# Performance work log

Hardware: AMD Instinct MI355X
Metric: run time of the kernel (lower is better)

## Reference

```python
import jax, jax.numpy as jnp
import numpy as np

B, S, T, D, V = 512, 128, 128, 512, 128  # batch, enc len, dec steps (=longest_smi), dim_model, output_size


def setup_inputs() -> dict:
    key = jax.random.key(0)
    ks = jax.random.split(key, 17)
    sc = 0.05
    return {
        "e_all": jax.random.normal(ks[0], (B, S, D), jnp.float32),
        "e_h": jax.random.normal(ks[1], (1, B, D), jnp.float32),
        "e_c": jax.random.normal(ks[2], (1, B, D), jnp.float32),
        "target": jax.random.randint(ks[3], (B, T), 0, T),
        # params (Linear weights stored [in, out], y = x @ W + b)
        "E": jax.random.normal(ks[4], (T, D), jnp.float32) * sc,        # Embedding(longest_smi, D)
        "Wa": jax.random.normal(ks[5], (D, D), jnp.float32) * sc,
        "ba": jnp.zeros((D,), jnp.float32),
        "Ua": jax.random.normal(ks[6], (D, D), jnp.float32) * sc,
        "bu": jnp.zeros((D,), jnp.float32),
        "Va": jax.random.normal(ks[7], (D, 1), jnp.float32) * sc,
        "bv": jnp.zeros((1,), jnp.float32),
        "W_ih": jax.random.normal(ks[8], (2 * D, 4 * D), jnp.float32) * sc,
        "b_ih": jnp.zeros((4 * D,), jnp.float32),
        "W_hh": jax.random.normal(ks[9], (D, 4 * D), jnp.float32) * sc,
        "b_hh": jnp.zeros((4 * D,), jnp.float32),
        "W_out": jax.random.normal(ks[10], (D, V), jnp.float32) * sc,
        "b_out": jnp.zeros((V,), jnp.float32),
    }


def reference(e_all, e_h, e_c, target, E, Wa, ba, Ua, bu, Va, bv,
              W_ih, b_ih, W_hh, b_hh, W_out, b_out):
    Bb = e_all.shape[0]
    # teacher forcing: step 0 input is token 0 (SOS), then target[:, :-1]
    idx = jnp.concatenate([jnp.zeros((Bb, 1), target.dtype), target[:, :-1]], axis=1)  # [B,T]
    emb_all = E[idx]                       # [B,T,D] (dropout is identity in eval)
    keys_proj = e_all @ Ua + bu            # Ua(keys), loop-invariant  [B,S,D]
    h0, c0 = e_h[0], e_c[0]                # [B,D]

    def step(carry, emb):
        h, c = carry
        q = (h + c) @ Wa + ba                                   # [B,D]  Wa(query)
        s = jnp.tanh(q[:, None, :] + keys_proj) @ Va + bv       # [B,S,1]
        w = jax.nn.softmax(s[..., 0], axis=-1)                  # [B,S]
        ctx = jnp.einsum('bs,bsd->bd', w, e_all)                # [B,D]
        x = jnp.concatenate([emb, ctx], axis=-1)                # [B,2D]
        g = x @ W_ih + b_ih + h @ W_hh + b_hh                   # [B,4D], torch gate order i,f,g,o
        i_, f_, g_, o_ = jnp.split(g, 4, axis=-1)
        c2 = jax.nn.sigmoid(f_) * c + jax.nn.sigmoid(i_) * jnp.tanh(g_)
        h2 = jax.nn.sigmoid(o_) * jnp.tanh(c2)
        out = h2 @ W_out + b_out                                # [B,V]
        return (h2, c2), (out, w)

    _, (outs, attns) = jax.lax.scan(step, (h0, c0), jnp.swapaxes(emb_all, 0, 1))
    outputs = jax.nn.log_softmax(jnp.swapaxes(outs, 0, 1), axis=-1)  # [B,T,V]
    cross_attn = jnp.swapaxes(attns, 0, 1)                           # [B,T,S]
    return outputs, cross_attn
```

## Files before the change

kernel.cpp:

```cpp
#include <hip/hip_runtime.h>

#define B_ 512
#define S_ 128
#define T_ 128
#define D_ 512
#define V_ 128
#define LDW 72

typedef __attribute__((ext_vector_type(8))) short s16x8;
typedef __attribute__((ext_vector_type(4))) short s16x4;
typedef __attribute__((ext_vector_type(4))) float f32x4;

__device__ __forceinline__ float b2f(unsigned short h) {
    union { unsigned int u; float f; } x; x.u = ((unsigned int)h) << 16; return x.f;
}
__device__ __forceinline__ unsigned short f2b(float f) {
    union { float f; unsigned int u; } x; x.f = f;
    unsigned int u = x.u; u += 0x7FFFu + ((u >> 16) & 1u);
    return (unsigned short)(u >> 16);
}
#if __has_builtin(__builtin_amdgcn_rcpf)
__device__ __forceinline__ float rcp_f(float x) { return __builtin_amdgcn_rcpf(x); }
#else
__device__ __forceinline__ float rcp_f(float x) { return 1.0f / x; }
#endif
__device__ __forceinline__ float sigm(float x) { return rcp_f(1.0f + __expf(-x)); }
__device__ __forceinline__ float tanh_fast(float x) {
    float e = __expf(2.0f * fabsf(x));
    float r = 1.0f - 2.0f * rcp_f(e + 1.0f);
    return copysignf(r, x);
}

struct P {
    const int* target;
    const float* E; const float* Va; const float* bv; const float* ba; const float* bout;
    const short* ealb; const short* kpb;
    const short* WaT; const short* WehT; const short* WctxT; const short* WoutT;
    const float* bcat;
    float* qb; short* xeh; short* ctxb; float* gp;
    short* hcbf; short* h2bf; float* cst;
    float* out_logits; float* out_attn;
};

struct AttnS { float sc[S_]; float wbuf[S_]; float red[2]; float cpart[4][D_]; };
struct GateS { short As[64][LDW]; short Bs[64][LDW]; float gt[64][68]; };
struct OutS  { short As[64][LDW]; short Bs[128][LDW]; };
union SharedU { AttnS a; GateS g; OutS o; };

__device__ __forceinline__ void attn_phase(const P& p, AttnS& sh, int b, int step)
{
    const int t = threadIdx.x, lane = t & 63, wave = t >> 6;
    const int d0 = lane * 8;
    float qr[8], var[8];
    const float* qrow = p.qb + (size_t)b * D_ + d0;
    #pragma unroll
    for (int j = 0; j < 8; ++j) { qr[j] = qrow[j]; var[j] = p.Va[d0 + j]; }
    const float bvv = p.bv[0];
    #pragma unroll 4
    for (int i = 0; i < 32; ++i) {
        int s = wave * 32 + i;
        s16x8 kv = *(const s16x8*)(p.kpb + ((size_t)b * S_ + s) * D_ + d0);
        float acc = 0.f;
        #pragma unroll
        for (int j = 0; j < 8; ++j)
            acc += tanh_fast(qr[j] + b2f((unsigned short)kv[j])) * var[j];
        #pragma unroll
        for (int o = 32; o >= 1; o >>= 1) acc += __shfl_xor(acc, o);
        if (lane == 0) sh.sc[s] = acc + bvv;
    }
    __syncthreads();
    if (wave == 0) {
        float v0 = sh.sc[lane], v1 = sh.sc[lane + 64];
        float m = fmaxf(v0, v1);
        #pragma unroll
        for (int o = 32; o >= 1; o >>= 1) m = fmaxf(m, __shfl_xor(m, o));
        float su = __expf(v0 - m) + __expf(v1 - m);
        #pragma unroll
        for (int o = 32; o >= 1; o >>= 1) su += __shfl_xor(su, o);
        if (lane == 0) { sh.red[0] = m; sh.red[1] = su; }
    }
    __syncthreads();
    {
        float m = sh.red[0], inv = rcp_f(sh.red[1]);
        if (t < S_) {
            float w = __expf(sh.sc[t] - m) * inv;
            sh.wbuf[t] = w;
            p.out_attn[((size_t)b * T_ + step) * S_ + t] = w;
        }
    }
    __syncthreads();
    {
        f32x4 aA = {0.f,0.f,0.f,0.f}, aB = {0.f,0.f,0.f,0.f};
        const short* eb = p.ealb + (size_t)b * S_ * D_ + d0;
        #pragma unroll 4
        for (int i = 0; i < 32; ++i) {
            int s = wave * 32 + i;
            float wv = sh.wbuf[s];
            s16x8 ev = *(const s16x8*)(eb + (size_t)s * D_);
            #pragma unroll
            for (int j = 0; j < 4; ++j) aA[j] += wv * b2f((unsigned short)ev[j]);
            #pragma unroll
            for (int j = 0; j < 4; ++j) aB[j] += wv * b2f((unsigned short)ev[4 + j]);
        }
        *(f32x4*)&sh.cpart[wave][d0]     = aA;
        *(f32x4*)&sh.cpart[wave][d0 + 4] = aB;
    }
    __syncthreads();
    {
        int dd = t * 2;
        float v0 = sh.cpart[0][dd]   + sh.cpart[1][dd]   + sh.cpart[2][dd]   + sh.cpart[3][dd];
        float v1 = sh.cpart[0][dd+1] + sh.cpart[1][dd+1] + sh.cpart[2][dd+1] + sh.cpart[3][dd+1];
        short2 o2; o2.x = (short)f2b(v0); o2.y = (short)f2b(v1);
        *(short2*)(p.ctxb + (size_t)b * D_ + dd) = o2;
    }
}

__device__ __forceinline__ void pgate_phase(const P& p, GateS& sh, int bid2)
{
    const int t = threadIdx.x, lane = t & 63, wave = t >> 6;
    const int wr = wave >> 1, wc = wave & 1;
    const int lrow = lane & 15, kq = lane >> 4;
    const int srow = t >> 3, sseg = t & 7;
    const int m0 = (bid2 >> 5) * 64, n0 = (bid2 & 31) * 64;
    const int K = 1024;
    f32x4 acc[2][2] = {};
    for (int k0 = 0; k0 < K; k0 += 64) {
        s16x8 va0 = *(const s16x8*)(p.xeh + (size_t)(m0 + srow) * K + k0 + sseg * 8);
        s16x8 va1 = *(const s16x8*)(p.xeh + (size_t)(m0 + srow + 32) * K + k0 + sseg * 8);
        s16x8 vb0 = *(const s16x8*)(p.WehT + (size_t)(n0 + srow) * K + k0 + sseg * 8);
        s16x8 vb1 = *(const s16x8*)(p.WehT + (size_t)(n0 + srow + 32) * K + k0 + sseg * 8);
        __syncthreads();
        *(s16x8*)(&sh.As[srow][sseg * 8]) = va0;
        *(s16x8*)(&sh.As[srow + 32][sseg * 8]) = va1;
        *(s16x8*)(&sh.Bs[srow][sseg * 8]) = vb0;
        *(s16x8*)(&sh.Bs[srow + 32][sseg * 8]) = vb1;
        __syncthreads();
        #pragma unroll
        for (int kk = 0; kk < 64; kk += 32) {
            s16x8 af0 = *(const s16x8*)(&sh.As[wr * 32 + lrow][kk + kq * 8]);
            s16x8 af1 = *(const s16x8*)(&sh.As[wr * 32 + 16 + lrow][kk + kq * 8]);
            s16x8 bf0 = *(const s16x8*)(&sh.Bs[wc * 32 + lrow][kk + kq * 8]);
            s16x8 bf1 = *(const s16x8*)(&sh.Bs[wc * 32 + 16 + lrow][kk + kq * 8]);
            acc[0][0] = __builtin_amdgcn_mfma_f32_16x16x32_bf16(af0, bf0, acc[0][0], 0, 0, 0);
            acc[0][1] = __builtin_amdgcn_mfma_f32_16x16x32_bf16(af0, bf1, acc[0][1], 0, 0, 0);
            acc[1][0] = __builtin_amdgcn_mfma_f32_16x16x32_bf16(af1, bf0, acc[1][0], 0, 0, 0);
            acc[1][1] = __builtin_amdgcn_mfma_f32_16x16x32_bf16(af1, bf1, acc[1][1], 0, 0, 0);
        }
    }
    #pragma unroll
    for (int m2 = 0; m2 < 2; ++m2)
        #pragma unroll
        for (int n2 = 0; n2 < 2; ++n2) {
            int cl = wc * 32 + n2 * 16 + lrow;
            float bvv = p.bcat[n0 + cl];
            #pragma unroll
            for (int j = 0; j < 4; ++j) {
                int rl = wr * 32 + m2 * 16 + kq * 4 + j;
                p.gp[(size_t)(m0 + rl) * 2048 + n0 + cl] = acc[m2][n2][j] + bvv;
            }
        }
}

__device__ __forceinline__ void fgate_phase(const P& p, GateS& sh, int bid, int step)
{
    const int t = threadIdx.x, lane = t & 63, wave = t >> 6;
    const int wr = wave >> 1, wc = wave & 1;
    const int lrow = lane & 15, kq = lane >> 4;
    const int srow = t >> 3, sseg = t & 7;
    const int m0 = (bid >> 5) * 64, n0 = (bid & 31) * 64;
    f32x4 acc[2][2] = {};
    for (int k0 = 0; k0 < 512; k0 += 64) {
        s16x8 va0 = *(const s16x8*)(p.ctxb + (size_t)(m0 + srow) * 512 + k0 + sseg * 8);
        s16x8 va1 = *(const s16x8*)(p.ctxb + (size_t)(m0 + srow + 32) * 512 + k0 + sseg * 8);
        s16x8 vb0 = *(const s16x8*)(p.WctxT + (size_t)(n0 + srow) * 512 + k0 + sseg * 8);
        s16x8 vb1 = *(const s16x8*)(p.WctxT + (size_t)(n0 + srow + 32) * 512 + k0 + sseg * 8);
        __syncthreads();
        *(s16x8*)(&sh.As[srow][sseg * 8]) = va0;
        *(s16x8*)(&sh.As[srow + 32][sseg * 8]) = va1;
        *(s16x8*)(&sh.Bs[srow][sseg * 8]) = vb0;
        *(s16x8*)(&sh.Bs[srow + 32][sseg * 8]) = vb1;
        __syncthreads();
        #pragma unroll
        for (int kk = 0; kk < 64; kk += 32) {
            s16x8 af0 = *(const s16x8*)(&sh.As[wr * 32 + lrow][kk + kq * 8]);
            s16x8 af1 = *(const s16x8*)(&sh.As[wr * 32 + 16 + lrow][kk + kq * 8]);
            s16x8 bf0 = *(const s16x8*)(&sh.Bs[wc * 32 + lrow][kk + kq * 8]);
            s16x8 bf1 = *(const s16x8*)(&sh.Bs[wc * 32 + 16 + lrow][kk + kq * 8]);
            acc[0][0] = __builtin_amdgcn_mfma_f32_16x16x32_bf16(af0, bf0, acc[0][0], 0, 0, 0);
            acc[0][1] = __builtin_amdgcn_mfma_f32_16x16x32_bf16(af0, bf1, acc[0][1], 0, 0, 0);
            acc[1][0] = __builtin_amdgcn_mfma_f32_16x16x32_bf16(af1, bf0, acc[1][0], 0, 0, 0);
            acc[1][1] = __builtin_amdgcn_mfma_f32_16x16x32_bf16(af1, bf1, acc[1][1], 0, 0, 0);
        }
    }
    #pragma unroll
    for (int m2 = 0; m2 < 2; ++m2)
        #pragma unroll
        for (int n2 = 0; n2 < 2; ++n2) {
            int cl = wc * 32 + n2 * 16 + lrow;
            #pragma unroll
            for (int j = 0; j < 4; ++j) {
                int rl = wr * 32 + m2 * 16 + kq * 4 + j;
                sh.gt[rl][cl] = acc[m2][n2][j] + p.gp[(size_t)(m0 + rl) * 2048 + n0 + cl];
            }
        }
    __syncthreads();
    const int rl4 = t >> 4, dl = t & 15;
    #pragma unroll
    for (int pass = 0; pass < 4; ++pass) {
        int row = pass * 16 + rl4;
        int b = m0 + row;
        int d = (n0 >> 2) + dl;
        float gi = sh.gt[row][dl * 4 + 0];
        float gf = sh.gt[row][dl * 4 + 1];
        float gg = sh.gt[row][dl * 4 + 2];
        float go = sh.gt[row][dl * 4 + 3];
        float cv = p.cst[(size_t)b * D_ + d];
        float c2 = sigm(gf) * cv + sigm(gi) * tanh_fast(gg);
        float h2 = sigm(go) * tanh_fast(c2);
        p.cst[(size_t)b * D_ + d] = c2;
        p.hcbf[(size_t)b * D_ + d] = (short)f2b(h2 + c2);
        p.h2bf[(size_t)b * D_ + d] = (short)f2b(h2);
        p.xeh[(size_t)b * 1024 + 512 + d] = (short)f2b(h2);
        int tok = p.target[b * T_ + step];
        p.xeh[(size_t)b * 1024 + d] = (short)f2b(p.E[(size_t)tok * D_ + d]);
    }
}

__device__ __forceinline__ void q_phase(const P& p, OutS& sh, int bid)
{
    const int t = threadIdx.x, lane = t & 63, wave = t >> 6;
    const int lrow = lane & 15, kq = lane >> 4;
    const int srow = t >> 3, sseg = t & 7;
    const int m0 = (bid >> 4) * 64, n0 = (bid & 15) * 32;
    f32x4 acc0 = {}, acc1 = {};
    for (int k0 = 0; k0 < 512; k0 += 64) {
        s16x8 va0 = *(const s16x8*)(p.hcbf + (size_t)(m0 + srow) * 512 + k0 + sseg * 8);
        s16x8 va1 = *(const s16x8*)(p.hcbf + (size_t)(m0 + srow + 32) * 512 + k0 + sseg * 8);
        s16x8 vb0 = *(const s16x8*)(p.WaT + (size_t)(n0 + srow) * 512 + k0 + sseg * 8);
        __syncthreads();
        *(s16x8*)(&sh.As[srow][sseg * 8]) = va0;
        *(s16x8*)(&sh.As[srow + 32][sseg * 8]) = va1;
        if (srow < 32) *(s16x8*)(&sh.Bs[srow][sseg * 8]) = vb0;
        __syncthreads();
        #pragma unroll
        for (int kk = 0; kk < 64; kk += 32) {
            s16x8 af  = *(const s16x8*)(&sh.As[wave * 16 + lrow][kk + kq * 8]);
            s16x8 bf0 = *(const s16x8*)(&sh.Bs[lrow][kk + kq * 8]);
            s16x8 bf1 = *(const s16x8*)(&sh.Bs[16 + lrow][kk + kq * 8]);
            acc0 = __builtin_amdgcn_mfma_f32_16x16x32_bf16(af, bf0, acc0, 0, 0, 0);
            acc1 = __builtin_amdgcn_mfma_f32_16x16x32_bf16(af, bf1, acc1, 0, 0, 0);
        }
    }
    #pragma unroll
    for (int n2 = 0; n2 < 2; ++n2) {
        int col = n0 + n2 * 16 + lrow;
        float bvv = p.ba[col];
        f32x4 av = n2 ? acc1 : acc0;
        #pragma unroll
        for (int j = 0; j < 4; ++j) {
            int row = m0 + wave * 16 + kq * 4 + j;
            p.qb[(size_t)row * 512 + col] = av[j] + bvv;
        }
    }
}

__device__ __forceinline__ void out_phase(const P& p, OutS& sh, int obid, int step)
{
    const int t = threadIdx.x, lane = t & 63, wave = t >> 6;
    const int lrow = lane & 15, kq = lane >> 4;
    const int srow = t >> 3, sseg = t & 7;
    const int m0 = obid * 64;
    f32x4 acc[8] = {};
    for (int k0 = 0; k0 < 512; k0 += 64) {
        s16x8 va0 = *(const s16x8*)(p.h2bf + (size_t)(m0 + srow) * 512 + k0 + sseg * 8);
        s16x8 va1 = *(const s16x8*)(p.h2bf + (size_t)(m0 + srow + 32) * 512 + k0 + sseg * 8);
        s16x8 vb[4];
        #pragma unroll
        for (int p4 = 0; p4 < 4; ++p4)
            vb[p4] = *(const s16x8*)(p.WoutT + (size_t)(srow + p4 * 32) * 512 + k0 + sseg * 8);
        __syncthreads();
        *(s16x8*)(&sh.As[srow][sseg * 8]) = va0;
        *(s16x8*)(&sh.As[srow + 32][sseg * 8]) = va1;
        #pragma unroll
        for (int p4 = 0; p4 < 4; ++p4) *(s16x8*)(&sh.Bs[srow + p4 * 32][sseg * 8]) = vb[p4];
        __syncthreads();
        #pragma unroll
        for (int kk = 0; kk < 64; kk += 32) {
            s16x8 a = *(const s16x8*)(&sh.As[wave * 16 + lrow][kk + kq * 8]);
            #pragma unroll
            for (int f = 0; f < 8; ++f) {
                s16x8 b = *(const s16x8*)(&sh.Bs[f * 16 + lrow][kk + kq * 8]);
                acc[f] = __builtin_amdgcn_mfma_f32_16x16x32_bf16(a, b, acc[f], 0, 0, 0);
            }
        }
    }
    float colb[8];
    #pragma unroll
    for (int f = 0; f < 8; ++f) colb[f] = p.bout[f * 16 + lrow];
    #pragma unroll
    for (int j = 0; j < 4; ++j) {
        float v[8]; float mx = -1e30f;
        #pragma unroll
        for (int f = 0; f < 8; ++f) { v[f] = acc[f][j] + colb[f]; mx = fmaxf(mx, v[f]); }
        #pragma unroll
        for (int o = 1; o < 16; o <<= 1) mx = fmaxf(mx, __shfl_xor(mx, o));
        float sum = 0.f;
        #pragma unroll
        for (int f = 0; f < 8; ++f) sum += __expf(v[f] - mx);
        #pragma unroll
        for (int o = 1; o < 16; o <<= 1) sum += __shfl_xor(sum, o);
        float lse = mx + __logf(sum);
        int row = m0 + wave * 16 + kq * 4 + j;
        float* orow = p.out_logits + ((size_t)row * T_ + step) * V_;
        #pragma unroll
        for (int f = 0; f < 8; ++f) orow[f * 16 + lrow] = v[f] - lse;
    }
}

__global__ __launch_bounds__(256, 2) void kA(P p, int step) {
    __shared__ SharedU sh;
    const int bid = blockIdx.x;
    if (bid < 512)       attn_phase(p, sh.a, bid, step);
    else if (bid < 768)  pgate_phase(p, sh.g, bid - 512);
    else if (step > 0)   out_phase(p, sh.o, bid - 768, step - 1);
}
__global__ __launch_bounds__(256, 2) void kB(P p, int step) {
    __shared__ SharedU sh;
    fgate_phase(p, sh.g, blockIdx.x, step);
}
__global__ __launch_bounds__(256, 2) void kC(P p) {
    __shared__ SharedU sh;
    q_phase(p, sh.o, blockIdx.x);
}
__global__ __launch_bounds__(256, 2) void kOutLast(P p, int step) {
    __shared__ SharedU sh;
    out_phase(p, sh.o, blockIdx.x, step);
}

template<bool OUT_BF16>
__global__ __launch_bounds__(256)
void gemm64(const short* __restrict__ A, const short* __restrict__ Bt,
            const float* __restrict__ bias, void* __restrict__ Cp,
            int M, int N, int K)
{
    __shared__ __align__(16) short As[64][LDW];
    __shared__ __align__(16) short Bs[64][LDW];
    const int t = threadIdx.x;
    const int lane = t & 63, wave = t >> 6;
    const int wr = wave >> 1, wc = wave & 1;
    const int lrow = lane & 15, kq = lane >> 4;
    const int m0 = blockIdx.y * 64, n0 = blockIdx.x * 64;
    const int srow = t >> 3, sseg = t & 7;
    f32x4 acc[2][2] = {};
    for (int k0 = 0; k0 < K; k0 += 64) {
        s16x8 va0 = *(const s16x8*)(A + (size_t)(m0 + srow) * K + k0 + sseg * 8);
        s16x8 va1 = *(const s16x8*)(A + (size_t)(m0 + srow + 32) * K + k0 + sseg * 8);
        s16x8 vb0 = *(const s16x8*)(Bt + (size_t)(n0 + srow) * K + k0 + sseg * 8);
        s16x8 vb1 = *(const s16x8*)(Bt + (size_t)(n0 + srow + 32) * K + k0 + sseg * 8);
        __syncthreads();
        *(s16x8*)(&As[srow][sseg * 8]) = va0;
        *(s16x8*)(&As[srow + 32][sseg * 8]) = va1;
        *(s16x8*)(&Bs[srow][sseg * 8]) = vb0;
        *(s16x8*)(&Bs[srow + 32][sseg * 8]) = vb1;
        __syncthreads();
        for (int kk = 0; kk < 64; kk += 32) {
            s16x8 af[2], bf[2];
            af[0] = *(const s16x8*)(&As[wr * 32 + lrow][kk + kq * 8]);
            af[1] = *(const s16x8*)(&As[wr * 32 + 16 + lrow][kk + kq * 8]);
            bf[0] = *(const s16x8*)(&Bs[wc * 32 + lrow][kk + kq * 8]);
            bf[1] = *(const s16x8*)(&Bs[wc * 32 + 16 + lrow][kk + kq * 8]);
            for (int m2 = 0; m2 < 2; ++m2)
                for (int n2 = 0; n2 < 2; ++n2)
                    acc[m2][n2] = __builtin_amdgcn_mfma_f32_16x16x32_bf16(af[m2], bf[n2], acc[m2][n2], 0, 0, 0);
        }
    }
    for (int m2 = 0; m2 < 2; ++m2)
        for (int n2 = 0; n2 < 2; ++n2) {
            int col = n0 + wc * 32 + n2 * 16 + lrow;
            float bvv = bias ? bias[col] : 0.0f;
            for (int j = 0; j < 4; ++j) {
                int row = m0 + wr * 32 + m2 * 16 + kq * 4 + j;
                float v = acc[m2][n2][j] + bvv;
                if (OUT_BF16) ((short*)Cp)[(size_t)row * N + col] = (short)f2b(v);
                else          ((float*)Cp)[(size_t)row * N + col] = v;
            }
        }
}

__global__ __launch_bounds__(256)
void init_state(const float* __restrict__ e_h, const float* __restrict__ e_c,
                float* __restrict__ c, short* __restrict__ hcbf,
                short* __restrict__ xeh, const float* __restrict__ E)
{
    int gid = blockIdx.x * 256 + threadIdx.x;
    int b = gid >> 9, d = gid & 511;
    float h0 = e_h[gid], c0 = e_c[gid];
    c[gid] = c0;
    hcbf[gid] = (short)f2b(h0 + c0);
    xeh[(size_t)b * 1024 + 512 + d] = (short)f2b(h0);
    xeh[(size_t)b * 1024 + d] = (short)f2b(E[d]);
}

__global__ __launch_bounds__(256)
void transpose_cast(const float* __restrict__ in, short* __restrict__ out,
                    int N, int ostride, int koff, int gate_perm)
{
    __shared__ float tile[64][65];
    int t = threadIdx.x;
    int n0 = blockIdx.x * 64, k0 = blockIdx.y * 64;
    int cc = t & 63, r4 = t >> 6;
    for (int i = 0; i < 16; ++i) {
        int r = i * 4 + r4;
        tile[r][cc] = in[(size_t)(k0 + r) * N + n0 + cc];
    }
    __syncthreads();
    for (int i = 0; i < 16; ++i) {
        int nr = i * 4 + r4;
        int ng = n0 + nr;
        int np = gate_perm ? ((ng & 511) * 4 + (ng >> 9)) : ng;
        out[(size_t)np * ostride + koff + k0 + cc] = (short)f2b(tile[cc][nr]);
    }
}

__global__ __launch_bounds__(256)
void cast_bf16_v4(const float* __restrict__ in, short* __restrict__ out, int n4)
{
    int i = blockIdx.x * 256 + threadIdx.x;
    int stride = gridDim.x * 256;
    for (; i < n4; i += stride) {
        f32x4 v = ((const f32x4*)in)[i];
        s16x4 o;
        for (int j = 0; j < 4; ++j) o[j] = (short)f2b(v[j]);
        ((s16x4*)out)[i] = o;
    }
}

__global__ __launch_bounds__(256)
void make_bcat(const float* __restrict__ b_ih, const float* __restrict__ b_hh, float* __restrict__ bcat)
{
    int i = blockIdx.x * 256 + threadIdx.x;
    if (i < 2048) {
        int np = (i & 511) * 4 + (i >> 9);
        bcat[np] = b_ih[i] + b_hh[i];
    }
}

extern "C" void kernel_launch(void* const* d_in, const int* in_sizes, int n_in,
                              void* d_out, int out_size, void* d_ws, size_t ws_size,
                              hipStream_t stream)
{
    const float* e_all  = (const float*)d_in[0];
    const float* e_h    = (const float*)d_in[1];
    const float* e_c    = (const float*)d_in[2];
    const int*   target = (const int*)d_in[3];
    const float* E      = (const float*)d_in[4];
    const float* Wa     = (const float*)d_in[5];
    const float* ba     = (const float*)d_in[6];
    const float* Ua     = (const float*)d_in[7];
    const float* bu     = (const float*)d_in[8];
    const float* Va     = (const float*)d_in[9];
    const float* bv     = (const float*)d_in[10];
    const float* W_ih   = (const float*)d_in[11];
    const float* b_ih   = (const float*)d_in[12];
    const float* W_hh   = (const float*)d_in[13];
    const float* b_hh   = (const float*)d_in[14];
    const float* W_out  = (const float*)d_in[15];
    const float* b_out  = (const float*)d_in[16];

    char* ws = (char*)d_ws;
    size_t off = 0;
    auto alloc = [&](size_t bytes) { void* p = ws + off; off += (bytes + 255) & ~255ull; return p; };
    short* ealb  = (short*)alloc((size_t)B_ * S_ * D_ * 2);
    short* kpb   = (short*)alloc((size_t)B_ * S_ * D_ * 2);
    short* WaT   = (short*)alloc((size_t)D_ * D_ * 2);
    short* UaT   = (short*)alloc((size_t)D_ * D_ * 2);
    short* WehT  = (short*)alloc((size_t)2048 * 1024 * 2);
    short* WctxT = (short*)alloc((size_t)2048 * 512 * 2);
    short* WoutT = (short*)alloc((size_t)V_ * D_ * 2);
    float* bcat  = (float*)alloc(2048 * 4);
    float* qb    = (float*)alloc((size_t)B_ * D_ * 4);
    short* xeh   = (short*)alloc((size_t)B_ * 1024 * 2);
    short* ctxb  = (short*)alloc((size_t)B_ * D_ * 2);
    float* gp    = (float*)alloc((size_t)B_ * 2048 * 4);
    short* hcbf  = (short*)alloc((size_t)B_ * D_ * 2);
    short* h2bf  = (short*)alloc((size_t)B_ * D_ * 2);
    float* cst   = (float*)alloc((size_t)B_ * D_ * 4);
    if (off > ws_size) return;

    float* out_logits = (float*)d_out;
    float* out_attn   = (float*)d_out + (size_t)B_ * T_ * V_;

    cast_bf16_v4<<<4096, 256, 0, stream>>>(e_all, ealb, B_ * S_ * D_ / 4);
    transpose_cast<<<dim3(8, 8),  256, 0, stream>>>(Wa,  WaT,  512,  512, 0, 0);
    transpose_cast<<<dim3(8, 8),  256, 0, stream>>>(Ua,  UaT,  512,  512, 0, 0);
    transpose_cast<<<dim3(32, 8), 256, 0, stream>>>(W_ih,                 WehT,  2048, 1024, 0,   1);
    transpose_cast<<<dim3(32, 8), 256, 0, stream>>>(W_ih + 512 * 2048,    WctxT, 2048, 512,  0,   1);
    transpose_cast<<<dim3(32, 8), 256, 0, stream>>>(W_hh,                 WehT,  2048, 1024, 512, 1);
    transpose_cast<<<dim3(2, 8),  256, 0, stream>>>(W_out, WoutT, 128, 512, 0, 0);
    make_bcat<<<8, 256, 0, stream>>>(b_ih, b_hh, bcat);
    gemm64<true><<<dim3(8, 1024), 256, 0, stream>>>(ealb, UaT, bu, kpb, B_ * S_, 512, 512);
    init_state<<<1024, 256, 0, stream>>>(e_h, e_c, cst, hcbf, xeh, E);
    gemm64<false><<<dim3(8, 8), 256, 0, stream>>>(hcbf, WaT, ba, qb, B_, 512, 512);

    P pp;
    pp.target = target; pp.E = E; pp.Va = Va; pp.bv = bv; pp.ba = ba; pp.bout = b_out;
    pp.ealb = ealb; pp.kpb = kpb; pp.WaT = WaT; pp.WehT = WehT; pp.WctxT = WctxT; pp.WoutT = WoutT;
    pp.bcat = bcat; pp.qb = qb; pp.xeh = xeh; pp.ctxb = ctxb; pp.gp = gp;
    pp.hcbf = hcbf; pp.h2bf = h2bf; pp.cst = cst;
    pp.out_logits = out_logits; pp.out_attn = out_attn;

    for (int t = 0; t < T_; ++t) {
        kA<<<776, 256, 0, stream>>>(pp, t);
        kB<<<256, 256, 0, stream>>>(pp, t);
        if (t < T_ - 1) kC<<<128, 256, 0, stream>>>(pp);
    }
    kOutLast<<<8, 256, 0, stream>>>(pp, T_ - 1);
    (void)n_in; (void)in_sizes; (void)out_size;
}
```

Before: 7.296 ms.

## Restructure attention scoring per-lane, enlarge pregate GEMM tiles, store query in bf16

The attention score loop now gives each lane one source position and half of D, so partial sums go through shared memory instead of a 64-wide shuffle reduction per position. The softmax normalisation is folded into the first wave, which removes one block barrier. The query vector and Va are stored in bf16, halving their loads. The pregate GEMM moves from 64x64 to 128x128 tiles (64 blocks instead of 256) with a 4x4 MFMA accumulator per wave, trading more register pressure and fewer parallel blocks for better operand reuse. Rounding q to bf16 adds some precision loss.

```diff
diff --git a/kernel.cpp b/kernel.cpp
--- a/kernel.cpp
+++ b/kernel.cpp
@@ -33,63 +33,64 @@
 
 struct P {
     const int* target;
-    const float* E; const float* Va; const float* bv; const float* ba; const float* bout;
+    const float* E; const float* bv; const float* ba; const float* bout;
+    const short* vab;
     const short* ealb; const short* kpb;
     const short* WaT; const short* WehT; const short* WctxT; const short* WoutT;
     const float* bcat;
-    float* qb; short* xeh; short* ctxb; float* gp;
+    short* qbf; short* xeh; short* ctxb; float* gp;
     short* hcbf; short* h2bf; float* cst;
     float* out_logits; float* out_attn;
 };
 
-struct AttnS { float sc[S_]; float wbuf[S_]; float red[2]; float cpart[4][D_]; };
-struct GateS { short As[64][LDW]; short Bs[64][LDW]; float gt[64][68]; };
+struct AttnS { float scp[4][64]; float wbuf[S_]; float cpart[4][D_]; };
+struct PG128 { short As[128][LDW]; short Bs[128][LDW]; };
 struct OutS  { short As[64][LDW]; short Bs[128][LDW]; };
-union SharedU { AttnS a; GateS g; OutS o; };
+union SharedA { AttnS a; PG128 g; OutS o; };
 
 __device__ __forceinline__ void attn_phase(const P& p, AttnS& sh, int b, int step)
 {
     const int t = threadIdx.x, lane = t & 63, wave = t >> 6;
-    const int d0 = lane * 8;
-    float qr[8], var[8];
-    const float* qrow = p.qb + (size_t)b * D_ + d0;
-    #pragma unroll
-    for (int j = 0; j < 8; ++j) { qr[j] = qrow[j]; var[j] = p.Va[d0 + j]; }
-    const float bvv = p.bv[0];
-    #pragma unroll 4
-    for (int i = 0; i < 32; ++i) {
-        int s = wave * 32 + i;
-        s16x8 kv = *(const s16x8*)(p.kpb + ((size_t)b * S_ + s) * D_ + d0);
+    {
+        const int sg = wave & 1, dh = wave >> 1;
+        const int s = sg * 64 + lane;
+        const short* kr = p.kpb + ((size_t)b * S_ + s) * D_ + dh * 256;
+        const short* qv = p.qbf + (size_t)b * D_ + dh * 256;
+        const short* vv = p.vab + dh * 256;
         float acc = 0.f;
-        #pragma unroll
-        for (int j = 0; j < 8; ++j)
-            acc += tanh_fast(qr[j] + b2f((unsigned short)kv[j])) * var[j];
-        #pragma unroll
-        for (int o = 32; o >= 1; o >>= 1) acc += __shfl_xor(acc, o);
-        if (lane == 0) sh.sc[s] = acc + bvv;
+        #pragma unroll 4
+        for (int i = 0; i < 32; ++i) {
+            s16x8 kv = *(const s16x8*)(kr + i * 8);
+            s16x8 qk = *(const s16x8*)(qv + i * 8);
+            s16x8 vk = *(const s16x8*)(vv + i * 8);
+            #pragma unroll
+            for (int j = 0; j < 8; ++j)
+                acc += tanh_fast(b2f((unsigned short)qk[j]) + b2f((unsigned short)kv[j]))
+                       * b2f((unsigned short)vk[j]);
+        }
+        sh.scp[wave][lane] = acc;
     }
     __syncthreads();
     if (wave == 0) {
-        float v0 = sh.sc[lane], v1 = sh.sc[lane + 64];
+        const float bvv = p.bv[0];
+        float v0 = sh.scp[0][lane] + sh.scp[2][lane] + bvv;
+        float v1 = sh.scp[1][lane] + sh.scp[3][lane] + bvv;
         float m = fmaxf(v0, v1);
         #pragma unroll
         for (int o = 32; o >= 1; o >>= 1) m = fmaxf(m, __shfl_xor(m, o));
-        float su = __expf(v0 - m) + __expf(v1 - m);
+        float e0 = __expf(v0 - m), e1 = __expf(v1 - m);
+        float su = e0 + e1;
         #pragma unroll
         for (int o = 32; o >= 1; o >>= 1) su += __shfl_xor(su, o);
-        if (lane == 0) { sh.red[0] = m; sh.red[1] = su; }
+        float inv = rcp_f(su);
+        float w0 = e0 * inv, w1 = e1 * inv;
+        sh.wbuf[lane] = w0; sh.wbuf[lane + 64] = w1;
+        float* ao = p.out_attn + ((size_t)b * T_ + step) * S_;
+        ao[lane] = w0; ao[lane + 64] = w1;
     }
     __syncthreads();
     {
-        float m = sh.red[0], inv = rcp_f(sh.red[1]);
-        if (t < S_) {
-            float w = __expf(sh.sc[t] - m) * inv;
-            sh.wbuf[t] = w;
-            p.out_attn[((size_t)b * T_ + step) * S_ + t] = w;
-        }
-    }
-    __syncthreads();
-    {
+        const int d0 = lane * 8;
         f32x4 aA = {0.f,0.f,0.f,0.f}, aB = {0.f,0.f,0.f,0.f};
         const short* eb = p.ealb + (size_t)b * S_ * D_ + d0;
         #pragma unroll 4
@@ -115,51 +116,60 @@
     }
 }
 
-__device__ __forceinline__ void pgate_phase(const P& p, GateS& sh, int bid2)
+__device__ __forceinline__ void pgate_phase(const P& p, PG128& sh, int bid2)
 {
     const int t = threadIdx.x, lane = t & 63, wave = t >> 6;
     const int wr = wave >> 1, wc = wave & 1;
     const int lrow = lane & 15, kq = lane >> 4;
-    const int srow = t >> 3, sseg = t & 7;
-    const int m0 = (bid2 >> 5) * 64, n0 = (bid2 & 31) * 64;
+    const int m0 = (bid2 >> 4) * 128, n0 = (bid2 & 15) * 128;
     const int K = 1024;
-    f32x4 acc[2][2] = {};
+    f32x4 acc[4][4] = {};
     for (int k0 = 0; k0 < K; k0 += 64) {
-        s16x8 va0 = *(const s16x8*)(p.xeh + (size_t)(m0 + srow) * K + k0 + sseg * 8);
-        s16x8 va1 = *(const s16x8*)(p.xeh + (size_t)(m0 + srow + 32) * K + k0 + sseg * 8);
-        s16x8 vb0 = *(const s16x8*)(p.WehT + (size_t)(n0 + srow) * K + k0 + sseg * 8);
-        s16x8 vb1 = *(const s16x8*)(p.WehT + (size_t)(n0 + srow + 32) * K + k0 + sseg * 8);
-        __syncthreads();
-        *(s16x8*)(&sh.As[srow][sseg * 8]) = va0;
-        *(s16x8*)(&sh.As[srow + 32][sseg * 8]) = va1;
-        *(s16x8*)(&sh.Bs[srow][sseg * 8]) = vb0;
-        *(s16x8*)(&sh.Bs[srow + 32][sseg * 8]) = vb1;
+        s16x8 va[4], vb[4];
+        #pragma unroll
+        for (int r = 0; r < 4; ++r) {
+            int idx = r * 256 + t, row = idx >> 3, seg = idx & 7;
+            va[r] = *(const s16x8*)(p.xeh  + (size_t)(m0 + row) * K + k0 + seg * 8);
+            vb[r] = *(const s16x8*)(p.WehT + (size_t)(n0 + row) * K + k0 + seg * 8);
+        }
+        __syncthreads();
+        #pragma unroll
+        for (int r = 0; r < 4; ++r) {
+            int idx = r * 256 + t, row = idx >> 3, seg = idx & 7;
+            *(s16x8*)(&sh.As[row][seg * 8]) = va[r];
+            *(s16x8*)(&sh.Bs[row][seg * 8]) = vb[r];
+        }
         __syncthreads();
         #pragma unroll
         for (int kk = 0; kk < 64; kk += 32) {
-            s16x8 af0 = *(const s16x8*)(&sh.As[wr * 32 + lrow][kk + kq * 8]);
-            s16x8 af1 = *(const s16x8*)(&sh.As[wr * 32 + 16 + lrow][kk + kq * 8]);
-            s16x8 bf0 = *(const s16x8*)(&sh.Bs[wc * 32 + lrow][kk + kq * 8]);
-            s16x8 bf1 = *(const s16x8*)(&sh.Bs[wc * 32 + 16 + lrow][kk + kq * 8]);
-            acc[0][0] = __builtin_amdgcn_mfma_f32_16x16x32_bf16(af0, bf0, acc[0][0], 0, 0, 0);
-            acc[0][1] = __builtin_amdgcn_mfma_f32_16x16x32_bf16(af0, bf1, acc[0][1], 0, 0, 0);
-            acc[1][0] = __builtin_amdgcn_mfma_f32_16x16x32_bf16(af1, bf0, acc[1][0], 0, 0, 0);
-            acc[1][1] = __builtin_amdgcn_mfma_f32_16x16x32_bf16(af1, bf1, acc[1][1], 0, 0, 0);
+            s16x8 af[4], bf[4];
+            #pragma unroll
+            for (int f = 0; f < 4; ++f) {
+                af[f] = *(const s16x8*)(&sh.As[wr * 64 + f * 16 + lrow][kk + kq * 8]);
+                bf[f] = *(const s16x8*)(&sh.Bs[wc * 64 + f * 16 + lrow][kk + kq * 8]);
+            }
+            #pragma unroll
+            for (int fa = 0; fa < 4; ++fa)
+                #pragma unroll
+                for (int fb = 0; fb < 4; ++fb)
+                    acc[fa][fb] = __builtin_amdgcn_mfma_f32_16x16x32_bf16(af[fa], bf[fb], acc[fa][fb], 0, 0, 0);
         }
     }
     #pragma unroll
-    for (int m2 = 0; m2 < 2; ++m2)
-        #pragma unroll
-        for (int n2 = 0; n2 < 2; ++n2) {
-            int cl = wc * 32 + n2 * 16 + lrow;
-            float bvv = p.bcat[n0 + cl];
+    for (int fa = 0; fa < 4; ++fa)
+        #pragma unroll
+        for (int fb = 0; fb < 4; ++fb) {
+            int col = n0 + wc * 64 + fb * 16 + lrow;
+            float bvv = p.bcat[col];
             #pragma unroll
             for (int j = 0; j < 4; ++j) {
-                int rl = wr * 32 + m2 * 16 + kq * 4 + j;
-                p.gp[(size_t)(m0 + rl) * 2048 + n0 + cl] = acc[m2][n2][j] + bvv;
+                int row = m0 + wr * 64 + fa * 16 + kq * 4 + j;
+                p.gp[(size_t)row * 2048 + col] = acc[fa][fb][j] + bvv;
             }
         }
 }
+
+struct GateS { short As[64][LDW]; short Bs[64][LDW]; float gt[64][65]; };
 
 __device__ __forceinline__ void fgate_phase(const P& p, GateS& sh, int bid, int step)
 {
@@ -259,7 +269,7 @@
         #pragma unroll
         for (int j = 0; j < 4; ++j) {
             int row = m0 + wave * 16 + kq * 4 + j;
-            p.qb[(size_t)row * 512 + col] = av[j] + bvv;
+            p.qbf[(size_t)row * 512 + col] = (short)f2b(av[j] + bvv);
         }
     }
 }
@@ -318,23 +328,23 @@
 }
 
 __global__ __launch_bounds__(256, 2) void kA(P p, int step) {
-    __shared__ SharedU sh;
+    __shared__ SharedA sh;
     const int bid = blockIdx.x;
     if (bid < 512)       attn_phase(p, sh.a, bid, step);
-    else if (bid < 768)  pgate_phase(p, sh.g, bid - 512);
-    else if (step > 0)   out_phase(p, sh.o, bid - 768, step - 1);
+    else if (bid < 576)  pgate_phase(p, sh.g, bid - 512);
+    else if (step > 0)   out_phase(p, sh.o, bid - 576, step - 1);
 }
 __global__ __launch_bounds__(256, 2) void kB(P p, int step) {
-    __shared__ SharedU sh;
-    fgate_phase(p, sh.g, blockIdx.x, step);
+    __shared__ GateS sh;
+    fgate_phase(p, sh, blockIdx.x, step);
 }
 __global__ __launch_bounds__(256, 2) void kC(P p) {
-    __shared__ SharedU sh;
-    q_phase(p, sh.o, blockIdx.x);
+    __shared__ OutS sh;
+    q_phase(p, sh, blockIdx.x);
 }
 __global__ __launch_bounds__(256, 2) void kOutLast(P p, int step) {
-    __shared__ SharedU sh;
-    out_phase(p, sh.o, blockIdx.x, step);
+    __shared__ OutS sh;
+    out_phase(p, sh, blockIdx.x, step);
 }
 
 template<bool OUT_BF16>
@@ -478,7 +488,8 @@
     short* WctxT = (short*)alloc((size_t)2048 * 512 * 2);
     short* WoutT = (short*)alloc((size_t)V_ * D_ * 2);
     float* bcat  = (float*)alloc(2048 * 4);
-    float* qb    = (float*)alloc((size_t)B_ * D_ * 4);
+    short* qbf   = (short*)alloc((size_t)B_ * D_ * 2);
+    short* vab   = (short*)alloc((size_t)D_ * 2);
     short* xeh   = (short*)alloc((size_t)B_ * 1024 * 2);
     short* ctxb  = (short*)alloc((size_t)B_ * D_ * 2);
     float* gp    = (float*)alloc((size_t)B_ * 2048 * 4);
@@ -491,26 +502,28 @@
     float* out_attn   = (float*)d_out + (size_t)B_ * T_ * V_;
 
     cast_bf16_v4<<<4096, 256, 0, stream>>>(e_all, ealb, B_ * S_ * D_ / 4);
+    cast_bf16_v4<<<1,    256, 0, stream>>>(Va, vab, D_ / 4);
     transpose_cast<<<dim3(8, 8),  256, 0, stream>>>(Wa,  WaT,  512,  512, 0, 0);
     transpose_cast<<<dim3(8, 8),  256, 0, stream>>>(Ua,  UaT,  512,  512, 0, 0);
-    transpose_cast<<<dim3(32, 8), 256, 0, stream>>>(W_ih,                 WehT,  2048, 1024, 0,   1);
-    transpose_cast<<<dim3(32, 8), 256, 0, stream>>>(W_ih + 512 * 2048,    WctxT, 2048, 512,  0,   1);
-    transpose_cast<<<dim3(32, 8), 256, 0, stream>>>(W_hh,                 WehT,  2048, 1024, 512, 1);
+    transpose_cast<<<dim3(32, 8), 256, 0, stream>>>(W_ih,              WehT,  2048, 1024, 0,   1);
+    transpose_cast<<<dim3(32, 8), 256, 0, stream>>>(W_ih + 512 * 2048, WctxT, 2048, 512,  0,   1);
+    transpose_cast<<<dim3(32, 8), 256, 0, stream>>>(W_hh,              WehT,  2048, 1024, 512, 1);
     transpose_cast<<<dim3(2, 8),  256, 0, stream>>>(W_out, WoutT, 128, 512, 0, 0);
     make_bcat<<<8, 256, 0, stream>>>(b_ih, b_hh, bcat);
     gemm64<true><<<dim3(8, 1024), 256, 0, stream>>>(ealb, UaT, bu, kpb, B_ * S_, 512, 512);
     init_state<<<1024, 256, 0, stream>>>(e_h, e_c, cst, hcbf, xeh, E);
-    gemm64<false><<<dim3(8, 8), 256, 0, stream>>>(hcbf, WaT, ba, qb, B_, 512, 512);
+    gemm64<true><<<dim3(8, 8), 256, 0, stream>>>(hcbf, WaT, ba, qbf, B_, 512, 512);
 
     P pp;
-    pp.target = target; pp.E = E; pp.Va = Va; pp.bv = bv; pp.ba = ba; pp.bout = b_out;
+    pp.target = target; pp.E = E; pp.bv = bv; pp.ba = ba; pp.bout = b_out;
+    pp.vab = vab;
     pp.ealb = ealb; pp.kpb = kpb; pp.WaT = WaT; pp.WehT = WehT; pp.WctxT = WctxT; pp.WoutT = WoutT;
-    pp.bcat = bcat; pp.qb = qb; pp.xeh = xeh; pp.ctxb = ctxb; pp.gp = gp;
+    pp.bcat = bcat; pp.qbf = qbf; pp.xeh = xeh; pp.ctxb = ctxb; pp.gp = gp;
     pp.hcbf = hcbf; pp.h2bf = h2bf; pp.cst = cst;
     pp.out_logits = out_logits; pp.out_attn = out_attn;
 
     for (int t = 0; t < T_; ++t) {
-        kA<<<776, 256, 0, stream>>>(pp, t);
+        kA<<<584, 256, 0, stream>>>(pp, t);
         kB<<<256, 256, 0, stream>>>(pp, t);
         if (t < T_ - 1) kC<<<128, 256, 0, stream>>>(pp);
     }
```

Measured after the change: 7.442 ms. 1.02x slower.
